# Optimization experiments

Measured on AMD Instinct MI355X. Metric: run time of the kernel, lower is better.

## Reference

```python
import jax, jax.numpy as jnp
import numpy as np

N = 200000   # active voxels
C = 128      # in_channels == out_channels -> identity downsample
K = 27       # 3x3x3 kernel offsets
EPS = 1e-5


def setup_inputs() -> dict:
    key = jax.random.key(0)
    ks = jax.random.split(key, 4)
    x = jax.random.normal(ks[0], (N, C), jnp.float32)
    nbr = jax.random.randint(ks[1], (N, K), 0, N, jnp.int32)
    W1 = jax.random.normal(ks[2], (K, C, C), jnp.float32) * 0.05
    W2 = jax.random.normal(ks[3], (K, C, C), jnp.float32) * 0.05
    g1 = jnp.ones((C,), jnp.float32); b1 = jnp.zeros((C,), jnp.float32)
    g2 = jnp.ones((C,), jnp.float32); b2 = jnp.zeros((C,), jnp.float32)
    return {"x": x, "nbr": nbr, "W1": W1, "g1": g1, "b1": b1,
            "W2": W2, "g2": g2, "b2": b2}


def _sparse_conv(x, nbr, W):
    # gather-matmul-scatter sparse conv: out[i] = sum_k W[k]^T x[nbr[i,k]]
    # scan over the K=27 kernel offsets to avoid materializing [N,K,C].
    def body(acc, kn):
        Wk, nk = kn                               # [C,C], [N]
        return acc + jnp.take(x, nk, axis=0) @ Wk, None
    acc0 = jnp.zeros((x.shape[0], W.shape[2]), x.dtype)
    out, _ = jax.lax.scan(body, acc0, (W, nbr.T))
    return out


def _bn(x, g, b):
    # training-mode batch norm over the point dimension
    m = jnp.mean(x, axis=0)
    v = jnp.var(x, axis=0)
    return (x - m) * jax.lax.rsqrt(v + EPS) * g + b


def reference(x, nbr, W1, g1, b1, W2, g2, b2):
    out = jax.nn.relu(_bn(_sparse_conv(x, nbr, W1), g1, b1))
    out = _bn(_sparse_conv(out, nbr, W2), g2, b2)
    # downsample is identity (in_channels == out_channels, stride == 1)
    return jax.nn.relu(out + x)
```

## Files before the change

### kernel.cpp

```cpp
#include <hip/hip_runtime.h>
#include <hip/hip_bf16.h>
#include <stdint.h>

#define C_DIM 128
#define K_DIM 27

typedef __attribute__((ext_vector_type(8))) short short8;
typedef __attribute__((ext_vector_type(4))) float f32x4;
typedef __attribute__((ext_vector_type(4))) unsigned short ushort4v;

#define FENCE() asm volatile("" ::: "memory")
#define VMCNT0() asm volatile("s_waitcnt vmcnt(0)" ::: "memory")
#define LGKM0() asm volatile("s_waitcnt lgkmcnt(0)" ::: "memory")
#define BAR() __builtin_amdgcn_s_barrier()

__device__ __forceinline__ unsigned short f2bf(float f) {
  unsigned int u = __builtin_bit_cast(unsigned int, f);
  u += 0x7fffu + ((u >> 16) & 1u);
  return (unsigned short)(u >> 16);
}
__device__ __forceinline__ float bf2f(unsigned short h) {
  unsigned int u = ((unsigned int)h) << 16;
  return __builtin_bit_cast(float, u);
}

__device__ __forceinline__ void async_copy16(const void* gsrc, void* ldst) {
  __builtin_amdgcn_global_load_lds(
      (const __attribute__((address_space(1))) unsigned int*)gsrc,
      (__attribute__((address_space(3))) unsigned int*)ldst, 16, 0, 0);
}

__global__ __launch_bounds__(256) void prep_kernel(
    const float* __restrict__ W1, const float* __restrict__ W2,
    unsigned short* __restrict__ Wt1, unsigned short* __restrict__ Wt2,
    float* __restrict__ stats, int stats_n) {
  int idx = blockIdx.x * 256 + threadIdx.x;
  const int total = K_DIM * C_DIM * C_DIM;
  if (idx < total) {
    int e = idx & 7;
    int s = (idx >> 3) & 7;
    int co = (idx >> 6) & 127;
    int h = (idx >> 13) & 1;
    int k = idx >> 14;
    int ci = h * 64 + ((s ^ (co & 7)) << 3) + e;
    int src = (k * C_DIM + ci) * C_DIM + co;
    Wt1[idx] = f2bf(W1[src]);
    Wt2[idx] = f2bf(W2[src]);
  }
  if (idx < stats_n) stats[idx] = 0.f;
}

__global__ __launch_bounds__(256) void cvt_x_kernel(
    const float* __restrict__ x, unsigned short* __restrict__ xb, int total4) {
  int i = blockIdx.x * 256 + threadIdx.x;
  if (i >= total4) return;
  f32x4 v = ((const f32x4*)x)[i];
  ushort4v u;
#pragma unroll
  for (int j = 0; j < 4; ++j) u[j] = f2bf(v[j]);
  ((ushort4v*)xb)[i] = u;
}

template<int OUT_IS_F32>
__global__ __launch_bounds__(256, 2) void conv_kernel(
    const unsigned short* __restrict__ xb, const int* __restrict__ nbr,
    const unsigned short* __restrict__ Wt, void* __restrict__ out_v,
    float* __restrict__ stats, int N) {
  extern __shared__ __align__(16) char smem[];
  unsigned short* Wbuf = (unsigned short*)smem;
  unsigned short* Abuf = (unsigned short*)(smem + 32768);
  int* idx_lds = (int*)(smem + 65536);
  float* s_sum = (float*)(smem + 65536 + 13824);
  float* s_ssum = s_sum + C_DIM;

  const int tid = threadIdx.x;
  const int wave = tid >> 6, lane = tid & 63;
  const int lr = lane & 15, lg = lane >> 4;
  const int rg = wave >> 1, cg = wave & 1;
  const int row0 = blockIdx.x * 128;

  if (tid < C_DIM) { s_sum[tid] = 0.f; s_ssum[tid] = 0.f; }

  for (int i = tid; i < 128 * K_DIM; i += 256) {
    int r = i / K_DIM;
    int k = i - r * K_DIM;
    int rr = row0 + r; if (rr >= N) rr = N - 1;
    idx_lds[i] = nbr[(size_t)rr * K_DIM + k];
  }
  __syncthreads();

  const int sr = lane >> 3, g = lane & 7;

  auto stage_a = [&](const int (&gi)[4], int h, int buf) {
    unsigned short* dst = Abuf + buf * 8192 + wave * 2048;
#pragma unroll
    for (int c = 0; c < 4; ++c) {
      const unsigned short* src =
          xb + (size_t)gi[c] * C_DIM + h * 64 + ((g ^ (sr & 7)) << 3);
      async_copy16(src, dst + c * 512);
    }
  };
  auto stage_w = [&](int p, int buf) {
    const unsigned short* src = Wt + (size_t)p * 8192 + wave * 2048 + lane * 8;
    unsigned short* dst = Wbuf + buf * 8192 + wave * 2048;
#pragma unroll
    for (int c = 0; c < 4; ++c)
      async_copy16(src + c * 512, dst + c * 512);
  };
  auto read_gi = [&](int k, int (&gi)[4]) {
#pragma unroll
    for (int c = 0; c < 4; ++c)
      gi[c] = idx_lds[(wave * 32 + c * 8 + sr) * K_DIM + k];
  };

  f32x4 acc[4][4] = {};

  auto compute = [&](int buf) {
    const unsigned short* ab = Abuf + buf * 8192;
    const unsigned short* wb = Wbuf + buf * 8192;
    __builtin_amdgcn_s_setprio(1);
#pragma unroll
    for (int cs = 0; cs < 2; ++cs) {
      const int slot = ((cs * 4 + lg) ^ (lr & 7)) << 3;
      short8 a[4], b[4];
#pragma unroll
      for (int rt = 0; rt < 4; ++rt)
        a[rt] = *(const short8*)(ab + (rg * 64 + rt * 16 + lr) * 64 + slot);
#pragma unroll
      for (int ct = 0; ct < 4; ++ct)
        b[ct] = *(const short8*)(wb + (cg * 64 + ct * 16 + lr) * 64 + slot);
#pragma unroll
      for (int rt = 0; rt < 4; ++rt)
#pragma unroll
        for (int ct = 0; ct < 4; ++ct)
          acc[rt][ct] = __builtin_amdgcn_mfma_f32_16x16x32_bf16(a[rt], b[ct], acc[rt][ct], 0, 0, 0);
    }
    __builtin_amdgcn_s_setprio(0);
  };

  int giC[4], giN[4];
  read_gi(0, giC);
  LGKM0();
  stage_a(giC, 0, 0);
  stage_w(0, 0);
  LGKM0();
  VMCNT0();
  BAR();

  const int NP = K_DIM * 2;
#pragma unroll 2
  for (int p = 0; p < NP; ++p) {
    const int k = p >> 1, h = p & 1, cur = p & 1;
    if (p + 1 < NP) {
      if (h == 0) {
        stage_a(giC, 1, cur ^ 1);
        stage_w(p + 1, cur ^ 1);
        read_gi(k + 1 < K_DIM ? k + 1 : k, giN);
      } else {
        stage_a(giN, 0, cur ^ 1);
        stage_w(p + 1, cur ^ 1);
#pragma unroll
        for (int c = 0; c < 4; ++c) giC[c] = giN[c];
      }
    }
    FENCE();
    compute(cur);
    LGKM0();
    VMCNT0();
    BAR();
  }

  float* ctile = (float*)smem;
  float ps[4] = {0.f, 0.f, 0.f, 0.f}, pss[4] = {0.f, 0.f, 0.f, 0.f};
#pragma unroll
  for (int rt = 0; rt < 4; ++rt) {
#pragma unroll
    for (int j = 0; j < 4; ++j) {
      int lrow = rg * 64 + rt * 16 + lg * 4 + j;
      bool ok = (row0 + lrow) < N;
#pragma unroll
      for (int ct = 0; ct < 4; ++ct) {
        float v = acc[rt][ct][j];
        ctile[lrow * C_DIM + cg * 64 + ct * 16 + lr] = v;
        if (ok) { ps[ct] += v; pss[ct] += v * v; }
      }
    }
  }
#pragma unroll
  for (int ct = 0; ct < 4; ++ct) {
    ps[ct]  += __shfl_xor(ps[ct], 16, 64);
    ps[ct]  += __shfl_xor(ps[ct], 32, 64);
    pss[ct] += __shfl_xor(pss[ct], 16, 64);
    pss[ct] += __shfl_xor(pss[ct], 32, 64);
    if (lg == 0) {
      int col = cg * 64 + ct * 16 + lr;
      atomicAdd(&s_sum[col], ps[ct]);
      atomicAdd(&s_ssum[col], pss[ct]);
    }
  }
  __syncthreads();
  if (tid < C_DIM) {
    atomicAdd(&stats[tid], s_sum[tid]);
    atomicAdd(&stats[C_DIM + tid], s_ssum[tid]);
  }
  for (int i = tid; i < 4096; i += 256) {
    int row = i >> 5;
    int c4 = i & 31;
    int grow = row0 + row;
    if (grow >= N) continue;
    f32x4 v = ((const f32x4*)ctile)[i];
    if (OUT_IS_F32) {
      ((f32x4*)out_v)[(size_t)grow * 32 + c4] = v;
    } else {
      ushort4v u;
#pragma unroll
      for (int j = 0; j < 4; ++j) u[j] = f2bf(v[j]);
      ((ushort4v*)out_v)[(size_t)grow * 32 + c4] = u;
    }
  }
}

__global__ void finalize_kernel(const float* __restrict__ stats,
                                const float* __restrict__ g,
                                const float* __restrict__ b,
                                float* __restrict__ sshift, float invN) {
  int c = threadIdx.x;
  float mean = stats[c] * invN;
  float var = stats[128 + c] * invN - mean * mean;
  float sc = g[c] * rsqrtf(var + 1e-5f);
  sshift[c] = sc;
  sshift[128 + c] = b[c] - mean * sc;
}

__global__ __launch_bounds__(256) void apply_kernel(
    unsigned short* __restrict__ y, const float* __restrict__ ss, int total8) {
  int i = blockIdx.x * 256 + threadIdx.x;
  if (i >= total8) return;
  int cb = (i * 8) & 127;
  short8 u = ((short8*)y)[i];
#pragma unroll
  for (int j = 0; j < 8; ++j) {
    float f = bf2f((unsigned short)u[j]) * ss[cb + j] + ss[128 + cb + j];
    u[j] = (short)f2bf(fmaxf(f, 0.f));
  }
  ((short8*)y)[i] = u;
}

__global__ __launch_bounds__(256) void final_kernel(
    float* __restrict__ y2, const float* __restrict__ x,
    const float* __restrict__ ss, int total4) {
  int i = blockIdx.x * 256 + threadIdx.x;
  if (i >= total4) return;
  int cb = (i * 4) & 127;
  f32x4 v = ((const f32x4*)y2)[i];
  f32x4 xv = ((const f32x4*)x)[i];
#pragma unroll
  for (int j = 0; j < 4; ++j)
    v[j] = fmaxf(v[j] * ss[cb + j] + ss[128 + cb + j] + xv[j], 0.f);
  ((f32x4*)y2)[i] = v;
}

extern "C" void kernel_launch(void* const* d_in, const int* in_sizes, int n_in,
                              void* d_out, int out_size, void* d_ws, size_t ws_size,
                              hipStream_t stream) {
  const float* x  = (const float*)d_in[0];
  const int* nbr  = (const int*)d_in[1];
  const float* W1 = (const float*)d_in[2];
  const float* g1 = (const float*)d_in[3];
  const float* b1 = (const float*)d_in[4];
  const float* W2 = (const float*)d_in[5];
  const float* g2 = (const float*)d_in[6];
  const float* b2 = (const float*)d_in[7];
  float* out = (float*)d_out;

  const int N = in_sizes[0] / C_DIM;
  const int totalW = K_DIM * C_DIM * C_DIM;
  const int SMEM_BYTES = 65536 + 13824 + 1024;

  char* ws = (char*)d_ws;
  size_t off = 0;
  auto alloc = [&](size_t bytes) {
    void* p = ws + off;
    off = (off + bytes + 255) & ~(size_t)255;
    return p;
  };
  unsigned short* Wt1 = (unsigned short*)alloc((size_t)totalW * 2);
  unsigned short* Wt2 = (unsigned short*)alloc((size_t)totalW * 2);
  float* stats = (float*)alloc(512 * 4);
  float* ss1   = (float*)alloc(256 * 4);
  float* ss2   = (float*)alloc(256 * 4);
  unsigned short* y1 = (unsigned short*)alloc((size_t)N * C_DIM * 2);
  unsigned short* xb_ws = (unsigned short*)alloc((size_t)N * C_DIM * 2);
  unsigned short* xb = (off <= ws_size) ? xb_ws : (unsigned short*)d_out;

  (void)hipFuncSetAttribute((const void*)conv_kernel<0>,
      hipFuncAttributeMaxDynamicSharedMemorySize, SMEM_BYTES);
  (void)hipFuncSetAttribute((const void*)conv_kernel<1>,
      hipFuncAttributeMaxDynamicSharedMemorySize, SMEM_BYTES);

  const int nblk = (N + 127) / 128;
  const float invN = 1.0f / (float)N;

  prep_kernel<<<(totalW + 255) / 256, 256, 0, stream>>>(W1, W2, Wt1, Wt2, stats, 512);

  {
    int t4 = N * C_DIM / 4;
    cvt_x_kernel<<<(t4 + 255) / 256, 256, 0, stream>>>(x, xb, t4);
  }

  conv_kernel<0><<<nblk, 256, SMEM_BYTES, stream>>>(xb, nbr, Wt1, y1, stats, N);
  finalize_kernel<<<1, 128, 0, stream>>>(stats, g1, b1, ss1, invN);

  {
    int t8 = N * C_DIM / 8;
    apply_kernel<<<(t8 + 255) / 256, 256, 0, stream>>>(y1, ss1, t8);
  }

  conv_kernel<1><<<nblk, 256, SMEM_BYTES, stream>>>(y1, nbr, Wt2, out, stats + 256, N);
  finalize_kernel<<<1, 128, 0, stream>>>(stats + 256, g2, b2, ss2, invN);

  {
    int t4 = N * C_DIM / 4;
    final_kernel<<<(t4 + 255) / 256, 256, 0, stream>>>(out, x, ss2, t4);
  }
}
```

Measured before the change: 609.0 us.

## Use four-stage 32-channel K-slice pipeline with partial vmcnt waits in sparse conv

Reorganizes the conv main loop from a double-buffered 64-channel pipeline into a four-buffer ring of 32-channel slices. Loads now run three stages ahead and the wait only drains down to vmcnt(8) instead of vmcnt(0), so gathered rows and weights stay in flight while MFMAs execute. The weight prep layout and LDS addressing change to match the 32-wide slices, and the XOR swizzle is dropped. The risks are LDS bank conflicts from the unswizzled 64-byte rows, twice as many barriers per offset, and lower MFMA work per sync.

```diff
diff --git a/kernel.cpp b/kernel.cpp
--- a/kernel.cpp
+++ b/kernel.cpp
@@ -9,7 +9,8 @@
 typedef __attribute__((ext_vector_type(4))) float f32x4;
 typedef __attribute__((ext_vector_type(4))) unsigned short ushort4v;
 
-#define FENCE() asm volatile("" ::: "memory")
+#define VMCNT8() asm volatile("s_waitcnt vmcnt(8)" ::: "memory")
+#define VMCNT4() asm volatile("s_waitcnt vmcnt(4)" ::: "memory")
 #define VMCNT0() asm volatile("s_waitcnt vmcnt(0)" ::: "memory")
 #define LGKM0() asm volatile("s_waitcnt lgkmcnt(0)" ::: "memory")
 #define BAR() __builtin_amdgcn_s_barrier()
@@ -37,12 +38,11 @@
   int idx = blockIdx.x * 256 + threadIdx.x;
   const int total = K_DIM * C_DIM * C_DIM;
   if (idx < total) {
-    int e = idx & 7;
-    int s = (idx >> 3) & 7;
-    int co = (idx >> 6) & 127;
-    int h = (idx >> 13) & 1;
-    int k = idx >> 14;
-    int ci = h * 64 + ((s ^ (co & 7)) << 3) + e;
+    int cq = idx & 31;
+    int co = (idx >> 5) & 127;
+    int q  = (idx >> 12) & 3;
+    int k  = idx >> 14;
+    int ci = q * 32 + cq;
     int src = (k * C_DIM + ci) * C_DIM + co;
     Wt1[idx] = f2bf(W1[src]);
     Wt2[idx] = f2bf(W2[src]);
@@ -67,8 +67,8 @@
     const unsigned short* __restrict__ Wt, void* __restrict__ out_v,
     float* __restrict__ stats, int N) {
   extern __shared__ __align__(16) char smem[];
-  unsigned short* Wbuf = (unsigned short*)smem;
-  unsigned short* Abuf = (unsigned short*)(smem + 32768);
+  unsigned short* Abuf = (unsigned short*)smem;
+  unsigned short* Wbuf = (unsigned short*)(smem + 32768);
   int* idx_lds = (int*)(smem + 65536);
   float* s_sum = (float*)(smem + 65536 + 13824);
   float* s_ssum = s_sum + C_DIM;
@@ -89,87 +89,79 @@
   }
   __syncthreads();
 
-  const int sr = lane >> 3, g = lane & 7;
-
-  auto stage_a = [&](const int (&gi)[4], int h, int buf) {
-    unsigned short* dst = Abuf + buf * 8192 + wave * 2048;
-#pragma unroll
-    for (int c = 0; c < 4; ++c) {
-      const unsigned short* src =
-          xb + (size_t)gi[c] * C_DIM + h * 64 + ((g ^ (sr & 7)) << 3);
-      async_copy16(src, dst + c * 512);
-    }
+  const int gr = wave * 32 + (lane >> 2);
+  const int gcol = (lane & 3) * 8;
+
+  auto stage_a = [&](int gA, int gB, int q, int buf) {
+    unsigned short* dst = Abuf + buf * 4096 + wave * 1024;
+    async_copy16(xb + (size_t)gA * C_DIM + q * 32 + gcol, dst);
+    async_copy16(xb + (size_t)gB * C_DIM + q * 32 + gcol, dst + 512);
   };
   auto stage_w = [&](int p, int buf) {
-    const unsigned short* src = Wt + (size_t)p * 8192 + wave * 2048 + lane * 8;
-    unsigned short* dst = Wbuf + buf * 8192 + wave * 2048;
-#pragma unroll
-    for (int c = 0; c < 4; ++c)
-      async_copy16(src + c * 512, dst + c * 512);
+    const unsigned short* src = Wt + (size_t)p * 4096 + wave * 1024 + lane * 8;
+    unsigned short* dst = Wbuf + buf * 4096 + wave * 1024;
+    async_copy16(src, dst);
+    async_copy16(src + 512, dst + 512);
   };
-  auto read_gi = [&](int k, int (&gi)[4]) {
-#pragma unroll
-    for (int c = 0; c < 4; ++c)
-      gi[c] = idx_lds[(wave * 32 + c * 8 + sr) * K_DIM + k];
-  };
 
   f32x4 acc[4][4] = {};
 
   auto compute = [&](int buf) {
-    const unsigned short* ab = Abuf + buf * 8192;
-    const unsigned short* wb = Wbuf + buf * 8192;
+    const unsigned short* ab = Abuf + buf * 4096 + (rg * 64 + lr) * 32 + lg * 8;
+    const unsigned short* wb = Wbuf + buf * 4096 + (cg * 64 + lr) * 32 + lg * 8;
+    short8 a[4], b[4];
+#pragma unroll
+    for (int rt = 0; rt < 4; ++rt) a[rt] = *(const short8*)(ab + rt * 512);
+#pragma unroll
+    for (int ct = 0; ct < 4; ++ct) b[ct] = *(const short8*)(wb + ct * 512);
     __builtin_amdgcn_s_setprio(1);
 #pragma unroll
-    for (int cs = 0; cs < 2; ++cs) {
-      const int slot = ((cs * 4 + lg) ^ (lr & 7)) << 3;
-      short8 a[4], b[4];
-#pragma unroll
-      for (int rt = 0; rt < 4; ++rt)
-        a[rt] = *(const short8*)(ab + (rg * 64 + rt * 16 + lr) * 64 + slot);
+    for (int rt = 0; rt < 4; ++rt)
 #pragma unroll
       for (int ct = 0; ct < 4; ++ct)
-        b[ct] = *(const short8*)(wb + (cg * 64 + ct * 16 + lr) * 64 + slot);
-#pragma unroll
-      for (int rt = 0; rt < 4; ++rt)
-#pragma unroll
-        for (int ct = 0; ct < 4; ++ct)
-          acc[rt][ct] = __builtin_amdgcn_mfma_f32_16x16x32_bf16(a[rt], b[ct], acc[rt][ct], 0, 0, 0);
-    }
+        acc[rt][ct] = __builtin_amdgcn_mfma_f32_16x16x32_bf16(a[rt], b[ct], acc[rt][ct], 0, 0, 0);
     __builtin_amdgcn_s_setprio(0);
   };
 
-  int giC[4], giN[4];
-  read_gi(0, giC);
+  int gA = idx_lds[gr * K_DIM];
+  int gB = idx_lds[(gr + 16) * K_DIM];
   LGKM0();
-  stage_a(giC, 0, 0);
-  stage_w(0, 0);
-  LGKM0();
-  VMCNT0();
+  stage_a(gA, gB, 0, 0); stage_w(0, 0);
+  stage_a(gA, gB, 1, 1); stage_w(1, 1);
+  stage_a(gA, gB, 2, 2); stage_w(2, 2);
+  VMCNT8();
   BAR();
 
-  const int NP = K_DIM * 2;
-#pragma unroll 2
-  for (int p = 0; p < NP; ++p) {
-    const int k = p >> 1, h = p & 1, cur = p & 1;
-    if (p + 1 < NP) {
-      if (h == 0) {
-        stage_a(giC, 1, cur ^ 1);
-        stage_w(p + 1, cur ^ 1);
-        read_gi(k + 1 < K_DIM ? k + 1 : k, giN);
-      } else {
-        stage_a(giN, 0, cur ^ 1);
-        stage_w(p + 1, cur ^ 1);
-#pragma unroll
-        for (int c = 0; c < 4; ++c) giC[c] = giN[c];
-      }
-    }
-    FENCE();
-    compute(cur);
-    LGKM0();
-    VMCNT0();
-    BAR();
-  }
-
+  for (int base = 0; base < 104; base += 4) {
+    const int k1 = (base >> 2) + 1;
+    int hA, hB;
+    stage_a(gA, gB, 3, 3); stage_w(base + 3, 3);
+    hA = idx_lds[gr * K_DIM + k1];
+    hB = idx_lds[(gr + 16) * K_DIM + k1];
+    compute(0);
+    LGKM0(); VMCNT8(); BAR();
+    stage_a(hA, hB, 0, 0); stage_w(base + 4, 0);
+    compute(1);
+    LGKM0(); VMCNT8(); BAR();
+    stage_a(hA, hB, 1, 1); stage_w(base + 5, 1);
+    compute(2);
+    LGKM0(); VMCNT8(); BAR();
+    stage_a(hA, hB, 2, 2); stage_w(base + 6, 2);
+    compute(3);
+    LGKM0(); VMCNT8(); BAR();
+    gA = hA; gB = hB;
+  }
+
+  stage_a(gA, gB, 3, 3); stage_w(107, 3);
+  compute(0);
+  LGKM0(); VMCNT8(); BAR();
+  compute(1);
+  LGKM0(); VMCNT4(); BAR();
+  compute(2);
+  LGKM0(); VMCNT0(); BAR();
+  compute(3);
+
+  __syncthreads();
   float* ctile = (float*)smem;
   float ps[4] = {0.f, 0.f, 0.f, 0.f}, pss[4] = {0.f, 0.f, 0.f, 0.f};
 #pragma unroll
```

After: 582.9 us. 4.3% less time.
